# Optimization experiments

Hardware: AMD Instinct MI355X
Metric: run time of the kernel (lower is better)

The kernel has to match this reference:

```python
import jax, jax.numpy as jnp
from jax import lax
import numpy as np

KSIZE = 3        # patch-matching kernel
RATE = 2         # dilation/upsample rate
FUSE_K = 3       # fusion kernel size
SCALE = 10.0     # softmax scale
EPS = 1e-4


def _same_pads(size, k, s):
    # TF 'SAME' padding: total pad so out = ceil(size / s)
    out = -(-size // s)
    total = max(0, (out - 1) * s + k - size)
    top = total // 2
    return (top, total - top)


def _extract_patches(x, k, s):
    # x: [N,C,H,W] -> [N, L, C, k, k], SAME padding, row-major patch order
    ph = _same_pads(x.shape[2], k, s)
    pw = _same_pads(x.shape[3], k, s)
    p = lax.conv_general_dilated_patches(x, (k, k), (s, s), (ph, pw))
    N, _, Ho, Wo = p.shape
    C = x.shape[1]
    p = p.reshape(N, C, k, k, Ho * Wo)  # channel-major patch layout (matches torch unfold)
    return jnp.transpose(p, (0, 4, 1, 2, 3))


def setup_inputs() -> dict:
    key = jax.random.key(0)
    k1, k2 = jax.random.split(key)
    f = jax.random.normal(k1, (8, 96, 64, 64), dtype=jnp.float32)
    b = jax.random.normal(k2, (8, 96, 64, 64), dtype=jnp.float32)
    return {"f": f, "b": b}


def reference(f, b):
    # TF-style nearest-neighbor downsample (stride sampling)
    fs = f[:, :, ::RATE, ::RATE]
    bs = b[:, :, ::RATE, ::RATE]
    N, C, H, W = fs.shape  # downsampled dims; f and b share shape here
    L = H * W
    kernel = 2 * RATE

    # raw background patches for aggregation: [N, L, C, 2r, 2r]
    raw_w = _extract_patches(b, kernel, RATE)
    # matching patches from downsampled background: [N, L, C, 3, 3]
    w = _extract_patches(bs, KSIZE, 1)

    fuse_w = jnp.eye(FUSE_K, dtype=f.dtype).reshape(1, 1, FUSE_K, FUSE_K)
    ct_pad = kernel - 1 - 1  # conv_transpose padding=1 -> conv pad k-1-p = 2

    def attend(xi, wi, rwi):
        # xi: [C,H,W]; wi: [L,C,3,3]; rwi: [L,C,2r,2r]
        norm = jnp.sqrt(jnp.sum(wi * wi, axis=(1, 2, 3), keepdims=True))
        wn = wi / jnp.maximum(norm, EPS)
        # cosine-similarity correlation: [L,H,W]
        yi = lax.conv_general_dilated(xi[None], wn, (1, 1), ((1, 1), (1, 1)))[0]
        # fusion: identity-kernel convs over the [L_b, L_f] score map, both orientations
        y2 = yi.reshape(1, 1, L, L)
        y2 = lax.conv_general_dilated(y2, fuse_w, (1, 1), ((1, 1), (1, 1)))
        y2 = jnp.transpose(y2.reshape(H, W, H, W), (1, 0, 3, 2)).reshape(1, 1, L, L)
        y2 = lax.conv_general_dilated(y2, fuse_w, (1, 1), ((1, 1), (1, 1)))
        yi = jnp.transpose(y2.reshape(W, H, W, H), (1, 0, 3, 2)).reshape(L, H, W)
        # softmax over background patches (mask mm == 1 since mask is None)
        yi = jax.nn.softmax(yi * SCALE, axis=0)
        # conv_transpose2d(yi, rwi, stride=RATE, padding=1) / 4
        wct = jnp.flip(jnp.swapaxes(rwi, 0, 1), axis=(2, 3))  # [C, L, 2r, 2r]
        out = lax.conv_general_dilated(
            yi[None], wct, (1, 1), ((ct_pad, ct_pad), (ct_pad, ct_pad)),
            lhs_dilation=(RATE, RATE))[0]
        return out / 4.0

    y = jax.vmap(attend)(fs, w, raw_w)  # [N, C, H*RATE, W*RATE]
    return y.reshape(f.shape)
```

## Files before the change

kernel.cpp:

```cpp
#include <hip/hip_runtime.h>
#include <math.h>

#define NB 8
#define NC 96
#define HF 64
#define HS 32
#define L 1024
#define MN 1536

#define G_OFF    0ull
#define F1T_OFF  (8ull * 1024 * 1024)
#define YB_B     (64ull * 1024 * 1024)
#define RWT_B    (80ull * 1024 * 1024)
#define N_OFF    (27262976ull)
#define FS_OFF   (27271168ull)
#define BS_OFF   (28057600ull)
#define SQP_OFF  (28844032ull)
#define Z_OFF    0ull

typedef __attribute__((ext_vector_type(8))) short short8;
typedef __attribute__((ext_vector_type(4))) float float4v;

__device__ inline unsigned short f2bf(float x) {
    union { float f; unsigned u; } v; v.f = x;
    unsigned r = v.u + 0x7fff + ((v.u >> 16) & 1);
    return (unsigned short)(r >> 16);
}

__global__ void kprep(const float* __restrict__ f, const float* __restrict__ b,
                      float* __restrict__ ws) {
    int n = blockIdx.x, c = blockIdx.y, z = blockIdx.z;
    int t = threadIdx.x;
    __shared__ float pl[64][65];
    if (z == 0) {
        const float* src = f + ((size_t)n * NC + c) * (HF * HF);
        for (int e = 0; e < 16; ++e) {
            int idx = t + e * 256;
            pl[idx >> 6][idx & 63] = src[idx];
        }
        __syncthreads();
        float* dst = ws + FS_OFF + ((size_t)n * NC + c) * 1024;
        #pragma unroll
        for (int e = 0; e < 4; ++e) {
            int pos = t + e * 256;
            int i = pos >> 5, j = pos & 31;
            dst[pos] = pl[2 * i][2 * j];
        }
        return;
    }
    const float* bp = b + ((size_t)n * NC + c) * (HF * HF);
    for (int e = 0; e < 16; ++e) {
        int idx = t + e * 256;
        pl[idx >> 6][idx & 63] = bp[idx];
    }
    __syncthreads();
    float* bs = ws + BS_OFF + ((size_t)n * NC + c) * 1024;
    float* sqr = ws + SQP_OFF + ((size_t)n * NC + c) * 1024;
    #pragma unroll
    for (int e = 0; e < 4; ++e) {
        int pos = t + e * 256;
        int i = pos >> 5, j = pos & 31;
        float v = pl[2 * i][2 * j];
        bs[pos] = v;
        sqr[pos] = v * v;
    }
    unsigned short* RWtF = (unsigned short*)((char*)ws + RWT_B) + (size_t)n * MN * L
                           + (size_t)c * 32 * 512;
    int wv = t >> 6, ln = t & 63;
    int qd = ln >> 4, uv = ln & 15;
    int u = uv >> 2, v = uv & 3;
    #pragma unroll
    for (int it = 0; it < 8; ++it) {
        int kc = it * 4 + wv;
        short8 out8;
        int s = 2 * kc - 1 + v;
        bool sok = (s >= 0 && s < HF);
        #pragma unroll
        for (int j = 0; j < 8; ++j) {
            int ly = qd * 8 + j;
            int r = 2 * ly - 1 + u;
            float val = (sok && r >= 0 && r < HF) ? pl[r][s] : 0.f;
            out8[j] = (short)f2bf(val);
        }
        *(short8*)(RWtF + (size_t)kc * 512 + ln * 8) = out8;
    }
}

__global__ __launch_bounds__(256) void k1_gram(float* __restrict__ ws) {
    int n = blockIdx.x;
    int t = threadIdx.x;
    if (blockIdx.y == 8) {
        if (blockIdx.z != 0) return;
        __shared__ float sq[1024];
        #pragma unroll
        for (int e = 0; e < 4; ++e) {
            int pos = t + e * 256;
            float s = 0.f;
            for (int c = 0; c < NC; ++c)
                s += ws[SQP_OFF + ((size_t)n * NC + c) * 1024 + pos];
            sq[pos] = s;
        }
        __syncthreads();
        #pragma unroll
        for (int e = 0; e < 4; ++e) {
            int pos = t + e * 256;
            int i = pos >> 5, j = pos & 31;
            float nsq = 0.f;
            #pragma unroll
            for (int dy = -1; dy <= 1; ++dy)
                #pragma unroll
                for (int dx = -1; dx <= 1; ++dx) {
                    int ii = i + dy, jj = j + dx;
                    if (ii >= 0 && ii < HS && jj >= 0 && jj < HS) nsq += sq[ii * HS + jj];
                }
            ws[N_OFF + (size_t)n * L + pos] = 1.f / fmaxf(sqrtf(nsq), 1e-4f);
        }
        return;
    }
    int p0 = blockIdx.y * 128, l0 = blockIdx.z * 128;
    int tp = t >> 4, tm = t & 15;
    __shared__ float Bt[32][132];
    __shared__ float Ft[32][132];
    float acc[8][8] = {};
    const float* bsp = ws + BS_OFF + (size_t)n * NC * 1024;
    const float* fsp = ws + FS_OFF + (size_t)n * NC * 1024;
    for (int c0 = 0; c0 < NC; c0 += 32) {
        #pragma unroll
        for (int e = 0; e < 4; ++e) {
            int idx = t + e * 256;
            int cl = idx >> 5, vq = idx & 31;
            *(float4*)&Bt[cl][vq * 4] =
                *(const float4*)&bsp[(size_t)(c0 + cl) * 1024 + l0 + vq * 4];
            *(float4*)&Ft[cl][vq * 4] =
                *(const float4*)&fsp[(size_t)(c0 + cl) * 1024 + p0 + vq * 4];
        }
        __syncthreads();
        for (int cl = 0; cl < 32; ++cl) {
            float4 a0 = *(const float4*)&Bt[cl][tp * 8];
            float4 a1 = *(const float4*)&Bt[cl][tp * 8 + 4];
            float4 b0 = *(const float4*)&Ft[cl][tm * 8];
            float4 b1 = *(const float4*)&Ft[cl][tm * 8 + 4];
            float av[8] = {a0.x, a0.y, a0.z, a0.w, a1.x, a1.y, a1.z, a1.w};
            float bv[8] = {b0.x, b0.y, b0.z, b0.w, b1.x, b1.y, b1.z, b1.w};
            #pragma unroll
            for (int aa = 0; aa < 8; ++aa)
                #pragma unroll
                for (int bb = 0; bb < 8; ++bb)
                    acc[aa][bb] += av[aa] * bv[bb];
        }
        __syncthreads();
    }
    float* G = ws + G_OFF + (size_t)n * L * L;
    #pragma unroll
    for (int aa = 0; aa < 8; ++aa) {
        int l = l0 + tp * 8 + aa;
        *(float4*)&G[(size_t)l * L + p0 + tm * 8] =
            make_float4(acc[aa][0], acc[aa][1], acc[aa][2], acc[aa][3]);
        *(float4*)&G[(size_t)l * L + p0 + tm * 8 + 4] =
            make_float4(acc[aa][4], acc[aa][5], acc[aa][6], acc[aa][7]);
    }
}

__global__ __launch_bounds__(256) void k23_score_fuse1t(float* __restrict__ ws) {
    int bid = blockIdx.x;
    int n = bid & 7;
    int tile = bid >> 3;
    int i0 = (tile >> 5) * 32, j0 = (tile & 31) * 32;
    int t = threadIdx.x;
    __shared__ float U[36][37];
    __shared__ float sA[34][35];
    __shared__ float sinv[34];
    const float* G = ws + G_OFF + (size_t)n * L * L;
    const float* invn = ws + N_OFF + (size_t)n * L;
    if (t < 34) {
        int l = i0 - 1 + t;
        sinv[t] = ((unsigned)l < L) ? invn[l] : 0.f;
    }
    for (int e = 0; e < 6; ++e) {
        int idx = t + e * 256;
        if (idx < 1296) {
            int a = idx / 36, bq = idx - a * 36;
            int l = i0 - 2 + a, p = j0 - 2 + bq;
            float s = 0.f;
            #pragma unroll
            for (int dy = -1; dy <= 1; ++dy) {
                int ll = l + dy * 32, pp = p + dy * 32;
                if ((unsigned)ll < L && (unsigned)pp < L)
                    s += G[(size_t)ll * L + pp];
            }
            U[a][bq] = s;
        }
    }
    __syncthreads();
    for (int e = 0; e < 5; ++e) {
        int idx = t + e * 256;
        if (idx < 1156) {
            int ih = idx / 34, jh = idx - ih * 34;
            int l = i0 - 1 + ih, p = j0 - 1 + jh;
            float a = 0.f;
            if ((unsigned)l < L && (unsigned)p < L) {
                int lx = l & 31, px = p & 31;
                float s = 0.f;
                #pragma unroll
                for (int dx = -1; dx <= 1; ++dx) {
                    bool ok = (unsigned)(lx + dx) < HS && (unsigned)(px + dx) < HS;
                    float u = U[ih + 1 + dx][jh + 1 + dx];
                    s += ok ? u : 0.f;
                }
                a = sinv[ih] * s;
            }
            sA[ih][jh] = a;
        }
    }
    __syncthreads();
    float* F1T = ws + F1T_OFF + (size_t)n * L * L;
    #pragma unroll
    for (int e = 0; e < 4; ++e) {
        int idx = t + e * 256;
        int jl = idx >> 5, il = idx & 31;
        float v = sA[il][jl] + sA[il + 1][jl + 1] + sA[il + 2][jl + 2];
        F1T[(size_t)(j0 + jl) * L + i0 + il] = v;
    }
}

__global__ __launch_bounds__(256) void k4_fuse2_softmax(float* __restrict__ ws) {
    int n = blockIdx.x, px = blockIdx.y, py0 = blockIdx.z * 4;
    int t = threadIdx.x;
    __shared__ float trow[6][32][33];
    const float* F1T = ws + F1T_OFF + (size_t)n * L * L;
    int Jbase = px * HS + py0;
    #pragma unroll
    for (int e = 0; e < 6; ++e) {
        int idx = t + e * 256;
        int d = idx >> 8, q = idx & 255;
        int Jd = Jbase + d - 1;
        float4 v = make_float4(0.f, 0.f, 0.f, 0.f);
        if ((unsigned)Jd < L) {
            int rd = (Jd & 31) * HS + (Jd >> 5);
            v = *(const float4*)&F1T[(size_t)rd * L + 4 * q];
        }
        int col = q >> 3, r0 = (4 * q) & 31;
        trow[d][r0 + 0][col] = v.x;
        trow[d][r0 + 1][col] = v.y;
        trow[d][r0 + 2][col] = v.z;
        trow[d][r0 + 3][col] = v.w;
    }
    __syncthreads();
    int w = t >> 6, ln = t & 63;
    int py = py0 + w;
    int p = py * HS + px;
    float vals[16];
    float mymax = -1e30f;
    #pragma unroll
    for (int e = 0; e < 16; ++e) {
        int k = e * 64 + ln;
        float v = 0.f;
        #pragma unroll
        for (int d = 0; d < 3; ++d) {
            int kd = k + d - 1;
            if ((unsigned)kd < L) v += trow[w + d][kd >> 5][kd & 31];
        }
        v *= 10.0f;
        vals[e] = v;
        mymax = fmaxf(mymax, v);
    }
    #pragma unroll
    for (int off = 32; off > 0; off >>= 1)
        mymax = fmaxf(mymax, __shfl_xor(mymax, off));
    float mysum = 0.f;
    #pragma unroll
    for (int e = 0; e < 16; ++e) { vals[e] = __expf(vals[e] - mymax); mysum += vals[e]; }
    #pragma unroll
    for (int off = 32; off > 0; off >>= 1)
        mysum += __shfl_xor(mysum, off);
    float rinv = 1.f / mysum;
    unsigned short* YbF = (unsigned short*)((char*)ws + YB_B) + (size_t)n * L * L;
    int pt = p >> 4, fr = p & 15;
    #pragma unroll
    for (int e = 0; e < 16; ++e) {
        int k = e * 64 + ln;
        int kc = k >> 5, qd = (k >> 3) & 3, j = k & 7;
        YbF[((size_t)pt * 32 + kc) * 512 + (qd * 16 + fr) * 8 + j] = f2bf(vals[e] * rinv);
    }
}

__global__ __launch_bounds__(256) void k6_mfma_z(float* __restrict__ ws) {
    int n = blockIdx.x;
    int wv = threadIdx.x >> 6, lane = threadIdx.x & 63;
    int pt0 = blockIdx.z * 8 + (wv >> 1) * 4;
    int mt0 = blockIdx.y * 8 + (wv & 1) * 4;

    const unsigned short* YbF = (const unsigned short*)((const char*)ws + YB_B)
                                + (size_t)n * L * L + lane * 8;
    const unsigned short* RWtF = (const unsigned short*)((const char*)ws + RWT_B)
                                 + (size_t)n * MN * L + lane * 8;

    float4v acc[4][4] = {};
    short8 af[2][4], bf[2][4];
    #pragma unroll
    for (int a = 0; a < 4; ++a) {
        af[0][a] = *(const short8*)(YbF + ((size_t)(pt0 + a) * 32) * 512);
        bf[0][a] = *(const short8*)(RWtF + ((size_t)(mt0 + a) * 32) * 512);
    }
    for (int kc = 0; kc < 32; ++kc) {
        int cur = kc & 1, nxt = cur ^ 1;
        if (kc < 31) {
            #pragma unroll
            for (int a = 0; a < 4; ++a) {
                af[nxt][a] = *(const short8*)(YbF + ((size_t)(pt0 + a) * 32 + kc + 1) * 512);
                bf[nxt][a] = *(const short8*)(RWtF + ((size_t)(mt0 + a) * 32 + kc + 1) * 512);
            }
        }
        #pragma unroll
        for (int a = 0; a < 4; ++a)
            #pragma unroll
            for (int bq = 0; bq < 4; ++bq)
                acc[a][bq] = __builtin_amdgcn_mfma_f32_16x16x32_bf16(
                    af[cur][a], bf[cur][bq], acc[a][bq], 0, 0, 0);
    }

    int fr = lane & 15, qd = lane >> 4;
    float* Zp = ws + Z_OFF + (size_t)n * L * MN;
    #pragma unroll
    for (int a = 0; a < 4; ++a) {
        #pragma unroll
        for (int r = 0; r < 4; ++r) {
            int p = (pt0 + a) * 16 + qd * 4 + r;
            #pragma unroll
            for (int bq = 0; bq < 4; ++bq) {
                int m = (mt0 + bq) * 16 + fr;
                Zp[(size_t)p * MN + m] = acc[a][bq][r];
            }
        }
    }
}

__global__ __launch_bounds__(256) void k7_gather(const float* __restrict__ ws,
                                                 float* __restrict__ out) {
    int n = blockIdx.x, yq = blockIdx.y, c0 = blockIdx.z * 2;
    int t = threadIdx.x;
    int y0 = yq * 4;
    int ibase = (y0 >> 1) - 1;
    __shared__ float zs[128][33];
    const float* Zp = ws + Z_OFF + (size_t)n * L * MN;
    #pragma unroll
    for (int e = 0; e < 4; ++e) {
        int idx = t + e * 256;
        int pl = idx >> 3, q = idx & 7;
        int il = pl >> 5, j = pl & 31;
        int i = ibase + il;
        float4 v = make_float4(0.f, 0.f, 0.f, 0.f);
        if (i >= 0 && i < HS)
            v = *(const float4*)&Zp[(size_t)(i * HS + j) * MN + c0 * 16 + q * 4];
        zs[pl][q * 4 + 0] = v.x;
        zs[pl][q * 4 + 1] = v.y;
        zs[pl][q * 4 + 2] = v.z;
        zs[pl][q * 4 + 3] = v.w;
    }
    __syncthreads();
    int y = y0 + (t >> 6), x = t & 63;
    int ih = (y + 1) >> 1, jh = (x + 1) >> 1;
    float s0 = 0.f, s1 = 0.f;
    #pragma unroll
    for (int di = 0; di < 2; ++di) {
        int i = ih - di;
        if (i < 0 || i >= HS) continue;
        int u = y + 1 - 2 * i;
        int il = i - ibase;
        #pragma unroll
        for (int dj = 0; dj < 2; ++dj) {
            int j = jh - dj;
            if (j < 0 || j >= HS) continue;
            int v = x + 1 - 2 * j;
            s0 += zs[il * 32 + j][u * 4 + v];
            s1 += zs[il * 32 + j][16 + u * 4 + v];
        }
    }
    out[(((size_t)n * NC + c0) * HF + y) * HF + x] = 0.25f * s0;
    out[(((size_t)n * NC + c0 + 1) * HF + y) * HF + x] = 0.25f * s1;
}

extern "C" void kernel_launch(void* const* d_in, const int* in_sizes, int n_in,
                              void* d_out, int out_size, void* d_ws, size_t ws_size,
                              hipStream_t stream) {
    const float* f = (const float*)d_in[0];
    const float* b = (const float*)d_in[1];
    float* out = (float*)d_out;
    float* ws = (float*)d_ws;

    kprep<<<dim3(NB, NC, 2), 256, 0, stream>>>(f, b, ws);
    k1_gram<<<dim3(NB, 9, 8), 256, 0, stream>>>(ws);
    k23_score_fuse1t<<<8192, 256, 0, stream>>>(ws);
    k4_fuse2_softmax<<<dim3(NB, 32, 8), 256, 0, stream>>>(ws);
    k6_mfma_z<<<dim3(NB, 12, 8), 256, 0, stream>>>(ws);
    k7_gather<<<dim3(NB, 16, 48), 256, 0, stream>>>(ws, out);
}
```

Baseline: 195.2 us.

## Store intermediate Z as transposed bf16 and gather with vectorized loads

The MFMA output Z is now written in bf16 instead of fp32, transposed to [m][p] layout so each lane writes four consecutive p values as one 8-byte store. The gather kernel reads 8 bf16 values per load along p and expands them into shared memory. This halves the intermediate buffer's write and read traffic and makes stores more coalesced. The cost is reduced precision of the pre-aggregation values and possible LDS bank conflicts from the scattered shared writes.

```diff
diff --git a/kernel.cpp b/kernel.cpp
--- a/kernel.cpp
+++ b/kernel.cpp
@@ -16,7 +16,7 @@
 #define FS_OFF   (27271168ull)
 #define BS_OFF   (28057600ull)
 #define SQP_OFF  (28844032ull)
-#define Z_OFF    0ull
+#define ZT_B     0ull
 
 typedef __attribute__((ext_vector_type(8))) short short8;
 typedef __attribute__((ext_vector_type(4))) float float4v;
@@ -25,6 +25,10 @@
     union { float f; unsigned u; } v; v.f = x;
     unsigned r = v.u + 0x7fff + ((v.u >> 16) & 1);
     return (unsigned short)(r >> 16);
+}
+__device__ inline float bf2f(unsigned short h) {
+    union { unsigned u; float f; } v; v.u = ((unsigned)h) << 16;
+    return v.f;
 }
 
 __global__ void kprep(const float* __restrict__ f, const float* __restrict__ b,
@@ -320,17 +324,17 @@
     }
 
     int fr = lane & 15, qd = lane >> 4;
-    float* Zp = ws + Z_OFF + (size_t)n * L * MN;
+    unsigned short* Zt = (unsigned short*)((char*)ws + ZT_B) + (size_t)n * MN * L;
     #pragma unroll
     for (int a = 0; a < 4; ++a) {
-        #pragma unroll
-        for (int r = 0; r < 4; ++r) {
-            int p = (pt0 + a) * 16 + qd * 4 + r;
-            #pragma unroll
-            for (int bq = 0; bq < 4; ++bq) {
-                int m = (mt0 + bq) * 16 + fr;
-                Zp[(size_t)p * MN + m] = acc[a][bq][r];
-            }
+        int p = (pt0 + a) * 16 + qd * 4;
+        #pragma unroll
+        for (int bq = 0; bq < 4; ++bq) {
+            int m = (mt0 + bq) * 16 + fr;
+            unsigned v0 = (unsigned)f2bf(acc[a][bq][0]) | ((unsigned)f2bf(acc[a][bq][1]) << 16);
+            unsigned v1 = (unsigned)f2bf(acc[a][bq][2]) | ((unsigned)f2bf(acc[a][bq][3]) << 16);
+            uint2 pk; pk.x = v0; pk.y = v1;
+            *(uint2*)(Zt + (size_t)m * L + p) = pk;
         }
     }
 }
@@ -342,20 +346,23 @@
     int y0 = yq * 4;
     int ibase = (y0 >> 1) - 1;
     __shared__ float zs[128][33];
-    const float* Zp = ws + Z_OFF + (size_t)n * L * MN;
-    #pragma unroll
-    for (int e = 0; e < 4; ++e) {
-        int idx = t + e * 256;
-        int pl = idx >> 3, q = idx & 7;
-        int il = pl >> 5, j = pl & 31;
+    const unsigned short* Zt = (const unsigned short*)((const char*)ws + ZT_B)
+                               + (size_t)n * MN * L;
+    #pragma unroll
+    for (int e = 0; e < 2; ++e) {
+        int idx = t + e * 256;
+        int m_l = idx & 31;
+        int pc = idx >> 5;
+        int il = pc >> 2;
         int i = ibase + il;
-        float4 v = make_float4(0.f, 0.f, 0.f, 0.f);
+        int jb = (pc & 3) * 8;
+        short8 v = {};
         if (i >= 0 && i < HS)
-            v = *(const float4*)&Zp[(size_t)(i * HS + j) * MN + c0 * 16 + q * 4];
-        zs[pl][q * 4 + 0] = v.x;
-        zs[pl][q * 4 + 1] = v.y;
-        zs[pl][q * 4 + 2] = v.z;
-        zs[pl][q * 4 + 3] = v.w;
+            v = *(const short8*)&Zt[(size_t)(c0 * 16 + m_l) * L + i * HS + jb];
+        int pbase = il * 32 + jb;
+        #pragma unroll
+        for (int k = 0; k < 8; ++k)
+            zs[pbase + k][m_l] = bf2f((unsigned short)v[k]);
     }
     __syncthreads();
     int y = y0 + (t >> 6), x = t & 63;
```

Result: slower. 230.2 us (+17.9%).
